# Optimization experiments

Hardware: AMD Instinct MI355X
Metric: run time of the kernel (lower is better)

## Reference

```python
import jax, jax.numpy as jnp
import numpy as np

B, S, D_MODEL, H = 2, 2048, 768, 12
HD = D_MODEL // H  # head_dim = 64
EPS = 1e-5


def setup_inputs() -> dict:
    key = jax.random.key(0)
    ks = jax.random.split(key, 5)
    sc = 0.02
    return {
        "x": jax.random.normal(ks[0], (B, S, D_MODEL), dtype=jnp.float32),
        "Wproj_w": jax.random.normal(ks[1], (7 * D_MODEL, D_MODEL), dtype=jnp.float32) * sc,
        "Wproj_b": jax.random.normal(ks[2], (7 * D_MODEL,), dtype=jnp.float32) * sc,
        "gn_w": jnp.ones((D_MODEL,), dtype=jnp.float32),
        "gn_b": jnp.zeros((D_MODEL,), dtype=jnp.float32),
        "out_w": jax.random.normal(ks[3], (D_MODEL, D_MODEL), dtype=jnp.float32) * sc,
        "out_b": jax.random.normal(ks[4], (D_MODEL,), dtype=jnp.float32) * sc,
    }


def _time_swiglu(qkv):
    # qkv: [B, S, 7, H, D]
    q1, k1, q2, k2, q3, k3, v = [qkv[:, :, i] for i in range(7)]
    a1 = jnp.einsum('bthd,bshd->bhts', q1, k1)  # [B,H,S,S], raw scores, no softmax
    a2 = jnp.einsum('bthd,bshd->bhts', q2, k2)
    a3 = jnp.einsum('bthd,bshd->bhts', q3, k3)
    t1 = jax.nn.silu(jnp.einsum('bhts,bshd->bthd', a1, v))
    t2 = jnp.einsum('bhts,bshd->bthd', a2, v)
    return jnp.einsum('bhts,bshd->bthd', a3, t1 * t2)  # [B,S,H,D]


def _group_norm(ctx, gn_w, gn_b):
    # ctx: [B, S, D_MODEL]; torch applies GroupNorm(H, D_MODEL) over (B, C=D_MODEL, L=S)
    g = ctx.reshape(B, S, H, HD)
    mean = jnp.mean(g, axis=(1, 3), keepdims=True)          # per (batch, group) over (S, HD)
    var = jnp.var(g, axis=(1, 3), keepdims=True)
    g = (g - mean) * jax.lax.rsqrt(var + EPS)
    g = g.reshape(B, S, D_MODEL)
    return g * gn_w + gn_b


def reference(x, Wproj_w, Wproj_b, gn_w, gn_b, out_w, out_b):
    qkv = x @ Wproj_w.T + Wproj_b                  # [B,S,7*D_MODEL]
    qkv = qkv.reshape(B, S, 7, H, HD)
    ctx = _time_swiglu(qkv).reshape(B, S, D_MODEL)  # [B,S,D_MODEL]
    ctx = _group_norm(ctx, gn_w, gn_b)
    return ctx @ out_w.T + out_b
```

## Files before the change

kernel.cpp:

```cpp
#include <hip/hip_runtime.h>
#include <hip/hip_bf16.h>
#include <stdint.h>

typedef short short8 __attribute__((ext_vector_type(8)));
typedef float f32x4 __attribute__((ext_vector_type(4)));
typedef float f32x16 __attribute__((ext_vector_type(16)));
typedef unsigned short u16x4 __attribute__((ext_vector_type(4)));
typedef unsigned uint4v __attribute__((ext_vector_type(4)));

#define MFMA16 __builtin_amdgcn_mfma_f32_16x16x32_bf16
#define MFMA32 __builtin_amdgcn_mfma_f32_32x32x16_bf16

typedef unsigned int __attribute__((address_space(1))) as1_u32;
typedef unsigned int __attribute__((address_space(3))) as3_u32;
#define GLOAD16(gsrc, ldst) \
  __builtin_amdgcn_global_load_lds((const as1_u32*)(gsrc), (as3_u32*)(ldst), 16, 0, 0)

__device__ __forceinline__ unsigned short f2bf(float f) {
  __hip_bfloat16 h = __float2bfloat16(f);
  return *(unsigned short*)&h;
}
__device__ __forceinline__ unsigned pk2(float lo, float hi) {
  return ((unsigned)f2bf(hi) << 16) | (unsigned)f2bf(lo);
}
__device__ __forceinline__ void plswap(unsigned &a, unsigned &b) {
  asm volatile("v_permlane32_swap_b32 %0, %1" : "+v"(a), "+v"(b));
}

__device__ __forceinline__ short8 pv_frag(const f32x16* acc, int kc2) {
  int n = kc2 >> 1, c = kc2 & 1;
  int o0 = 2 * c, o1 = 2 * c + 1;
  unsigned x0 = pk2(acc[n][o0 * 4 + 0], acc[n][o0 * 4 + 1]);
  unsigned x1 = pk2(acc[n][o0 * 4 + 2], acc[n][o0 * 4 + 3]);
  unsigned y0 = pk2(acc[n][o1 * 4 + 0], acc[n][o1 * 4 + 1]);
  unsigned y1 = pk2(acc[n][o1 * 4 + 2], acc[n][o1 * 4 + 3]);
  plswap(x0, y0);
  plswap(x1, y1);
  uint4v fu; fu.x = x0; fu.y = x1; fu.z = y0; fu.w = y1;
  return __builtin_bit_cast(short8, fu);
}

__global__ __launch_bounds__(256) void cvt_bf16_4(const float* __restrict__ in,
                                                  unsigned short* __restrict__ out,
                                                  int n) {
  int i = (blockIdx.x * 256 + threadIdx.x) * 4;
  if (i >= n) return;
  f32x4 v = *(const f32x4*)(in + i);
  u16x4 o;
  o.x = f2bf(v.x); o.y = f2bf(v.y); o.z = f2bf(v.z); o.w = f2bf(v.w);
  *(u16x4*)(out + i) = o;
}

__global__ __launch_bounds__(256) void transp64(const unsigned short* __restrict__ src,
                                                int stride, int off,
                                                unsigned short* __restrict__ dst) {
  __shared__ __align__(16) unsigned short t[64 * 64];
  const int tid = threadIdx.x;
  const int tt = blockIdx.x, bh = blockIdx.y;
  const int b = bh / 12, h = bh % 12;
  const unsigned short* sbase = src + (size_t)(b * 2048 + tt * 64) * stride + h * 64 + off;
  for (int it = 0; it < 2; ++it) {
    int slot = it * 256 + tid, s = slot >> 3, j = slot & 7;
    short8 v = *(const short8*)(sbase + (size_t)s * stride + j * 8);
    int phys = (s + 8 * j) & 63;
    for (int e = 0; e < 8; ++e)
      t[(j * 8 + e) * 64 + phys] = ((unsigned short*)&v)[e];
  }
  __syncthreads();
  unsigned short* dbase = dst + (size_t)bh * 64 * 2048 + tt * 64;
  for (int it = 0; it < 2; ++it) {
    int slot = it * 256 + tid, d = slot >> 3, c = slot & 7;
    int pc = (c + (d >> 3)) & 7;
    short8 v = *(const short8*)(t + d * 64 + pc * 8);
    *(short8*)(dbase + (size_t)d * 2048 + c * 8) = v;
  }
}

template <bool OUT_BF16>
__global__ __launch_bounds__(256) void gemm_nt(const unsigned short* __restrict__ A,
                                               const unsigned short* __restrict__ Bm,
                                               const float* __restrict__ bias,
                                               void* __restrict__ Cout,
                                               int M, int N, int K) {
  __shared__ __align__(16) char smem[32768];
  char* As = smem;
  char* Bs = smem + 16384;
  const int tid = threadIdx.x;
  const int w = tid >> 6, l = tid & 63;
  const int wm = w >> 1, wn = w & 1;
  const int Row0 = blockIdx.y * 128, Col0 = blockIdx.x * 128;

  f32x4 z; z.x = 0.f; z.y = 0.f; z.z = 0.f; z.w = 0.f;
  f32x4 acc[4][4];
  for (int m = 0; m < 4; ++m)
    for (int n = 0; n < 4; ++n) acc[m][n] = z;

  for (int k0 = 0; k0 < K; k0 += 64) {
    for (int it = 0; it < 4; ++it) {
      int slot = it * 256 + tid;
      int row = slot >> 3, j = slot & 7;
      int gc = j ^ (row & 7);
      GLOAD16(A + (size_t)(Row0 + row) * K + k0 + gc * 8, As + slot * 16);
      GLOAD16(Bm + (size_t)(Col0 + row) * K + k0 + gc * 8, Bs + slot * 16);
    }
    __syncthreads();
    for (int kc = 0; kc < 2; ++kc) {
      int c = (l >> 4) + 4 * kc;
      short8 af[4], bf[4];
      for (int m = 0; m < 4; ++m) {
        int t = wm * 64 + m * 16 + (l & 15);
        af[m] = *(const short8*)(As + t * 128 + ((c ^ (t & 7)) * 16));
      }
      for (int n = 0; n < 4; ++n) {
        int t = wn * 64 + n * 16 + (l & 15);
        bf[n] = *(const short8*)(Bs + t * 128 + ((c ^ (t & 7)) * 16));
      }
      for (int m = 0; m < 4; ++m)
        for (int n = 0; n < 4; ++n)
          acc[m][n] = MFMA16(af[m], bf[n], acc[m][n], 0, 0, 0);
    }
    __syncthreads();
  }
  for (int n = 0; n < 4; ++n) {
    int col = Col0 + wn * 64 + n * 16 + (l & 15);
    float bv = bias[col];
    for (int m = 0; m < 4; ++m) {
      int rbase = Row0 + wm * 64 + m * 16 + (l >> 4) * 4;
      for (int r = 0; r < 4; ++r) {
        float v = acc[m][n][r] + bv;
        size_t idx = (size_t)(rbase + r) * N + col;
        if (OUT_BF16) ((unsigned short*)Cout)[idx] = f2bf(v);
        else          ((float*)Cout)[idx] = v;
      }
    }
  }
}

__global__ __launch_bounds__(256) void pass1(const unsigned short* __restrict__ qkv,
                                             const unsigned short* __restrict__ vt,
                                             unsigned short* __restrict__ u) {
  __shared__ __align__(16) char smem[49152];
  const int tid = threadIdx.x, w = tid >> 6, l = tid & 63;
  const int m = w & 1, sh = w >> 1;
  const int g5 = l >> 5, l31 = l & 31;
  const int tt = blockIdx.x, bh = blockIdx.y;
  const int b = bh / 12, h = bh % 12;

  short8 qf[2][4];
#pragma unroll
  for (int tb = 0; tb < 2; ++tb) {
    const unsigned short* qrow =
        qkv + (size_t)(b * 2048 + tt * 64 + tb * 32 + l31) * 5376 + h * 64 + m * 2 * 768;
#pragma unroll
    for (int kc = 0; kc < 4; ++kc)
      qf[tb][kc] = *(const short8*)(qrow + kc * 16 + g5 * 8);
  }

  f32x16 z16;
#pragma unroll
  for (int i = 0; i < 16; ++i) z16[i] = 0.f;
  f32x16 tacc[2][2];
  tacc[0][0] = z16; tacc[0][1] = z16; tacc[1][0] = z16; tacc[1][1] = z16;

  auto STAGE = [&](char* buf, int si) {
#pragma unroll
    for (int shs = 0; shs < 2; ++shs) {
      int s0 = shs * 1024 + si * 32;
      char* hb = buf + shs * 12288;
      {
        int row = tid >> 3, pc = tid & 7, gc = pc ^ (row & 7);
        const unsigned short* base =
            qkv + (size_t)(b * 2048 + s0 + row) * 5376 + h * 64 + gc * 8;
        GLOAD16(base + 768, hb + tid * 16);
        GLOAD16(base + 3 * 768, hb + 4096 + tid * 16);
      }
      {
        int row = tid >> 2, pc = tid & 3, gc = pc ^ ((row >> 1) & 3);
        GLOAD16(vt + (size_t)(bh * 64 + row) * 2048 + s0 + gc * 8,
                hb + 8192 + tid * 16);
      }
    }
  };

  STAGE(smem, 0);
  __syncthreads();
  for (int si = 0; si < 32; ++si) {
    const char* cur = smem + (si & 1) * 24576 + sh * 12288;
    if (si < 31) STAGE(smem + ((si + 1) & 1) * 24576, si + 1);
    const char* Ks = cur + m * 4096;
    const char* Vs = cur + 8192;

    short8 kreg[4], vreg[4];
#pragma unroll
    for (int kc = 0; kc < 4; ++kc)
      kreg[kc] = *(const short8*)(Ks + l31 * 128 + (((kc * 2 + g5) ^ (l31 & 7)) * 16));
#pragma unroll
    for (int kc2 = 0; kc2 < 2; ++kc2)
#pragma unroll
      for (int dn = 0; dn < 2; ++dn) {
        int drow = dn * 32 + l31, c = kc2 * 2 + g5;
        vreg[kc2 * 2 + dn] =
            *(const short8*)(Vs + drow * 64 + ((c ^ ((drow >> 1) & 3)) * 16));
      }

#pragma unroll
    for (int tb = 0; tb < 2; ++tb) {
      f32x16 a = z16;
#pragma unroll
      for (int kc = 0; kc < 4; ++kc)
        a = MFMA32(kreg[kc], qf[tb][kc], a, 0, 0, 0);
#pragma unroll
      for (int kc2 = 0; kc2 < 2; ++kc2) {
        short8 pa = pv_frag(&a, kc2);
#pragma unroll
        for (int dn = 0; dn < 2; ++dn)
          tacc[tb][dn] = MFMA32(pa, vreg[kc2 * 2 + dn], tacc[tb][dn], 0, 0, 0);
      }
    }
    __syncthreads();
  }

  float* ex = (float*)smem;
  if (sh == 1) {
#pragma unroll
    for (int tb = 0; tb < 2; ++tb)
#pragma unroll
      for (int dn = 0; dn < 2; ++dn)
#pragma unroll
        for (int qd = 0; qd < 4; ++qd) {
          f32x4 v;
          v.x = tacc[tb][dn][qd * 4 + 0]; v.y = tacc[tb][dn][qd * 4 + 1];
          v.z = tacc[tb][dn][qd * 4 + 2]; v.w = tacc[tb][dn][qd * 4 + 3];
          *(f32x4*)((char*)ex + m * 16384 + ((tb * 2 + dn) * 4 + qd) * 1024 + l * 16) = v;
        }
  }
  __syncthreads();
  if (sh == 0) {
#pragma unroll
    for (int tb = 0; tb < 2; ++tb)
#pragma unroll
      for (int dn = 0; dn < 2; ++dn)
#pragma unroll
        for (int qd = 0; qd < 4; ++qd) {
          f32x4 v = *(const f32x4*)((char*)ex + m * 16384 +
                                    ((tb * 2 + dn) * 4 + qd) * 1024 + l * 16);
          tacc[tb][dn][qd * 4 + 0] += v.x; tacc[tb][dn][qd * 4 + 1] += v.y;
          tacc[tb][dn][qd * 4 + 2] += v.z; tacc[tb][dn][qd * 4 + 3] += v.w;
        }
  }
  __syncthreads();
  if (sh == 0 && m == 1) {
#pragma unroll
    for (int tb = 0; tb < 2; ++tb)
#pragma unroll
      for (int dn = 0; dn < 2; ++dn)
#pragma unroll
        for (int qd = 0; qd < 4; ++qd) {
          f32x4 v;
          v.x = tacc[tb][dn][qd * 4 + 0]; v.y = tacc[tb][dn][qd * 4 + 1];
          v.z = tacc[tb][dn][qd * 4 + 2]; v.w = tacc[tb][dn][qd * 4 + 3];
          *(f32x4*)((char*)ex + ((tb * 2 + dn) * 4 + qd) * 1024 + l * 16) = v;
        }
  }
  __syncthreads();
  if (sh == 0 && m == 0) {
#pragma unroll
    for (int tb = 0; tb < 2; ++tb)
#pragma unroll
      for (int dn = 0; dn < 2; ++dn)
#pragma unroll
        for (int r = 0; r < 16; ++r) {
          float x2 = ex[((tb * 2 + dn) * 4 + (r >> 2)) * 256 + l * 4 + (r & 3)];
          int t = tt * 64 + tb * 32 + (r & 3) + 8 * (r >> 2) + 4 * g5;
          int d = dn * 32 + l31;
          float x1 = tacc[tb][dn][r];
          float uu = (x1 / (1.f + expf(-x1))) * x2;
          u[(size_t)(b * 2048 + t) * 768 + h * 64 + d] = f2bf(uu);
        }
  }
}

__global__ __launch_bounds__(256) void pass2(const unsigned short* __restrict__ qkv,
                                             const unsigned short* __restrict__ ut,
                                             float* __restrict__ ctx,
                                             float* __restrict__ partials) {
  __shared__ __align__(16) char smem[32768];
  const int tid = threadIdx.x, w = tid >> 6, l = tid & 63;
  const int g5 = l >> 5, l31 = l & 31;
  const int tt = blockIdx.x, bh = blockIdx.y;
  const int b = bh / 12, h = bh % 12;

  short8 qf[2][4];
#pragma unroll
  for (int tb = 0; tb < 2; ++tb) {
    const unsigned short* qrow =
        qkv + (size_t)(b * 2048 + tt * 64 + tb * 32 + l31) * 5376 + h * 64 + 4 * 768;
#pragma unroll
    for (int kc = 0; kc < 4; ++kc)
      qf[tb][kc] = *(const short8*)(qrow + kc * 16 + g5 * 8);
  }

  f32x16 z16;
#pragma unroll
  for (int i = 0; i < 16; ++i) z16[i] = 0.f;
  f32x16 ca[2][2];
  ca[0][0] = z16; ca[0][1] = z16; ca[1][0] = z16; ca[1][1] = z16;

  auto STAGE = [&](int si) {
#pragma unroll
    for (int qs = 0; qs < 4; ++qs) {
      int s0 = qs * 512 + si * 32;
      char* hb = smem + qs * 8192;
      {
        int row = tid >> 3, pc = tid & 7, gc = pc ^ (row & 7);
        GLOAD16(qkv + (size_t)(b * 2048 + s0 + row) * 5376 + h * 64 + 5 * 768 + gc * 8,
                hb + tid * 16);
      }
      {
        int row = tid >> 2, pc = tid & 3, gc = pc ^ ((row >> 1) & 3);
        GLOAD16(ut + (size_t)(bh * 64 + row) * 2048 + s0 + gc * 8,
                hb + 4096 + tid * 16);
      }
    }
  };

  for (int si = 0; si < 16; ++si) {
    STAGE(si);
    __syncthreads();
    const char* Ks = smem + w * 8192;
    const char* Us = Ks + 4096;

    short8 kreg[4], ureg[4];
#pragma unroll
    for (int kc = 0; kc < 4; ++kc)
      kreg[kc] = *(const short8*)(Ks + l31 * 128 + (((kc * 2 + g5) ^ (l31 & 7)) * 16));
#pragma unroll
    for (int kc2 = 0; kc2 < 2; ++kc2)
#pragma unroll
      for (int dn = 0; dn < 2; ++dn) {
        int drow = dn * 32 + l31, c = kc2 * 2 + g5;
        ureg[kc2 * 2 + dn] =
            *(const short8*)(Us + drow * 64 + ((c ^ ((drow >> 1) & 3)) * 16));
      }

#pragma unroll
    for (int tb = 0; tb < 2; ++tb) {
      f32x16 a = z16;
#pragma unroll
      for (int kc = 0; kc < 4; ++kc)
        a = MFMA32(kreg[kc], qf[tb][kc], a, 0, 0, 0);
#pragma unroll
      for (int kc2 = 0; kc2 < 2; ++kc2) {
        short8 pa = pv_frag(&a, kc2);
#pragma unroll
        for (int dn = 0; dn < 2; ++dn)
          ca[tb][dn] = MFMA32(pa, ureg[kc2 * 2 + dn], ca[tb][dn], 0, 0, 0);
      }
    }
    __syncthreads();
  }

  float* ex = (float*)smem;
  auto DUMP = [&](int region) {
#pragma unroll
    for (int tb = 0; tb < 2; ++tb)
#pragma unroll
      for (int dn = 0; dn < 2; ++dn)
#pragma unroll
        for (int qd = 0; qd < 4; ++qd) {
          f32x4 v;
          v.x = ca[tb][dn][qd * 4 + 0]; v.y = ca[tb][dn][qd * 4 + 1];
          v.z = ca[tb][dn][qd * 4 + 2]; v.w = ca[tb][dn][qd * 4 + 3];
          *(f32x4*)((char*)ex + region * 16384 + ((tb * 2 + dn) * 4 + qd) * 1024 + l * 16) = v;
        }
  };
  auto ACCUM = [&](int region) {
#pragma unroll
    for (int tb = 0; tb < 2; ++tb)
#pragma unroll
      for (int dn = 0; dn < 2; ++dn)
#pragma unroll
        for (int qd = 0; qd < 4; ++qd) {
          f32x4 v = *(const f32x4*)((char*)ex + region * 16384 +
                                    ((tb * 2 + dn) * 4 + qd) * 1024 + l * 16);
          ca[tb][dn][qd * 4 + 0] += v.x; ca[tb][dn][qd * 4 + 1] += v.y;
          ca[tb][dn][qd * 4 + 2] += v.z; ca[tb][dn][qd * 4 + 3] += v.w;
        }
  };
  if (w == 1) DUMP(0);
  if (w == 3) DUMP(1);
  __syncthreads();
  if (w == 0) ACCUM(0);
  if (w == 2) ACCUM(1);
  __syncthreads();
  if (w == 2) DUMP(0);
  __syncthreads();
  float psum = 0.f, psum2 = 0.f;
  if (w == 0) {
    ACCUM(0);
#pragma unroll
    for (int tb = 0; tb < 2; ++tb)
#pragma unroll
      for (int dn = 0; dn < 2; ++dn)
#pragma unroll
        for (int r = 0; r < 16; ++r) {
          int t = tt * 64 + tb * 32 + (r & 3) + 8 * (r >> 2) + 4 * g5;
          int d = dn * 32 + l31;
          float v = ca[tb][dn][r];
          ctx[(size_t)(b * 2048 + t) * 768 + h * 64 + d] = v;
          psum += v; psum2 += v * v;
        }
    for (int off = 32; off > 0; off >>= 1) {
      psum += __shfl_down(psum, off, 64);
      psum2 += __shfl_down(psum2, off, 64);
    }
    if (l == 0) {
      partials[(bh * 32 + tt) * 2] = psum;
      partials[(bh * 32 + tt) * 2 + 1] = psum2;
    }
  }
}

__global__ __launch_bounds__(64) void gn_finalize(const float* __restrict__ partials,
                                                  float* __restrict__ stats) {
  const int g = blockIdx.x;
  const int l = threadIdx.x;
  double s = 0.0, s2 = 0.0;
  if (l < 32) {
    s = (double)partials[(g * 32 + l) * 2];
    s2 = (double)partials[(g * 32 + l) * 2 + 1];
  }
  for (int off = 32; off > 0; off >>= 1) {
    s += __shfl_down(s, off, 64);
    s2 += __shfl_down(s2, off, 64);
  }
  if (l == 0) {
    const double N = 2048.0 * 64.0;
    double mean = s / N;
    double var = s2 / N - mean * mean;
    stats[g * 2] = (float)mean;
    stats[g * 2 + 1] = (float)(1.0 / sqrt(var + 1e-5));
  }
}

__global__ __launch_bounds__(256) void gn_apply(const float* __restrict__ ctx,
                                                const float* __restrict__ stats,
                                                const float* __restrict__ gw,
                                                const float* __restrict__ gb,
                                                unsigned short* __restrict__ outc) {
  int i = blockIdx.x * 256 + threadIdx.x;
  if (i >= 4096 * 768) return;
  int c = i % 768;
  int b = i / (2048 * 768);
  int g = b * 12 + (c >> 6);
  float v = (ctx[i] - stats[2 * g]) * stats[2 * g + 1];
  outc[i] = f2bf(v * gw[c] + gb[c]);
}

extern "C" void kernel_launch(void* const* d_in, const int* in_sizes, int n_in,
                              void* d_out, int out_size, void* d_ws, size_t ws_size,
                              hipStream_t stream) {
  const float* x   = (const float*)d_in[0];
  const float* Wpw = (const float*)d_in[1];
  const float* Wpb = (const float*)d_in[2];
  const float* gnw = (const float*)d_in[3];
  const float* gnb = (const float*)d_in[4];
  const float* ow  = (const float*)d_in[5];
  const float* ob  = (const float*)d_in[6];
  float* out = (float*)d_out;

  char* ws = (char*)d_ws;
  size_t off = 0;
  auto carve = [&](size_t bytes) {
    char* p = ws + off;
    off = (off + bytes + 255) & ~(size_t)255;
    return p;
  };
  unsigned short* xb   = (unsigned short*)carve((size_t)4096 * 768 * 2);
  unsigned short* wb   = (unsigned short*)carve((size_t)5376 * 768 * 2);
  unsigned short* owb  = (unsigned short*)carve((size_t)768 * 768 * 2);
  unsigned short* qkvb = (unsigned short*)carve((size_t)4096 * 5376 * 2);
  unsigned short* ub   = (unsigned short*)carve((size_t)4096 * 768 * 2);
  unsigned short* vtb  = (unsigned short*)carve((size_t)24 * 64 * 2048 * 2);
  unsigned short* utb  = (unsigned short*)carve((size_t)24 * 64 * 2048 * 2);
  float* ctx           = (float*)carve((size_t)4096 * 768 * 4);
  float* partials      = (float*)carve(24 * 32 * 2 * 4);
  float* stats         = (float*)carve(48 * 4);

  cvt_bf16_4<<<3072, 256, 0, stream>>>(x, xb, 4096 * 768);
  cvt_bf16_4<<<4032, 256, 0, stream>>>(Wpw, wb, 5376 * 768);
  cvt_bf16_4<<<576, 256, 0, stream>>>(ow, owb, 768 * 768);

  gemm_nt<true><<<dim3(42, 32), 256, 0, stream>>>(xb, wb, Wpb, qkvb, 4096, 5376, 768);
  transp64<<<dim3(32, 24), 256, 0, stream>>>(qkvb, 5376, 6 * 768, vtb);
  pass1<<<dim3(32, 24), 256, 0, stream>>>(qkvb, vtb, ub);
  transp64<<<dim3(32, 24), 256, 0, stream>>>(ub, 768, 0, utb);
  pass2<<<dim3(32, 24), 256, 0, stream>>>(qkvb, utb, ctx, partials);
  gn_finalize<<<24, 64, 0, stream>>>(partials, stats);
  gn_apply<<<12288, 256, 0, stream>>>(ctx, stats, gnw, gnb, xb);
  gemm_nt<false><<<dim3(6, 32), 256, 0, stream>>>(xb, owb, ob, out, 4096, 768, 768);
}
```

Baseline: 227.4 us.

## Double-buffer pass2 staging, hoist load pointers, swizzle GEMM tiles, raise MFMA priority

Pass2 gets a double-buffered LDS stage of 64KB, so global-to-LDS loads for the next chunk overlap compute on the current one instead of waiting on a synchronous load. Both attention passes now advance precomputed pointers rather than recomputing addresses on each stage. They also wrap the MFMA section in s_setprio. The GEMM remaps block indices with an 8-way swizzle to improve L2 locality. The larger LDS footprint may lower pass2 occupancy, and the swizzle assumes the block count divides by 8.

```diff
diff --git a/kernel.cpp b/kernel.cpp
--- a/kernel.cpp
+++ b/kernel.cpp
@@ -88,7 +88,11 @@
   const int tid = threadIdx.x;
   const int w = tid >> 6, l = tid & 63;
   const int wm = w >> 1, wn = w & 1;
-  const int Row0 = blockIdx.y * 128, Col0 = blockIdx.x * 128;
+  const int gx = gridDim.x;
+  const int lin = blockIdx.y * gx + blockIdx.x;
+  const int cpx = (gx * gridDim.y) >> 3;
+  const int swz = (lin & 7) * cpx + (lin >> 3);
+  const int Row0 = (swz / gx) * 128, Col0 = (swz % gx) * 128;
 
   f32x4 z; z.x = 0.f; z.y = 0.f; z.z = 0.f; z.w = 0.f;
   f32x4 acc[4][4];
@@ -162,31 +166,30 @@
   f32x16 tacc[2][2];
   tacc[0][0] = z16; tacc[0][1] = z16; tacc[1][0] = z16; tacc[1][1] = z16;
 
-  auto STAGE = [&](char* buf, int si) {
-#pragma unroll
-    for (int shs = 0; shs < 2; ++shs) {
-      int s0 = shs * 1024 + si * 32;
-      char* hb = buf + shs * 12288;
-      {
-        int row = tid >> 3, pc = tid & 7, gc = pc ^ (row & 7);
-        const unsigned short* base =
-            qkv + (size_t)(b * 2048 + s0 + row) * 5376 + h * 64 + gc * 8;
-        GLOAD16(base + 768, hb + tid * 16);
-        GLOAD16(base + 3 * 768, hb + 4096 + tid * 16);
-      }
-      {
-        int row = tid >> 2, pc = tid & 3, gc = pc ^ ((row >> 1) & 3);
-        GLOAD16(vt + (size_t)(bh * 64 + row) * 2048 + s0 + gc * 8,
-                hb + 8192 + tid * 16);
-      }
-    }
+  const unsigned short *k1p0, *k1p1, *vtp0, *vtp1;
+  {
+    int row = tid >> 3, pc = tid & 7, gc = pc ^ (row & 7);
+    k1p0 = qkv + (size_t)(b * 2048 + row) * 5376 + h * 64 + 768 + gc * 8;
+    k1p1 = k1p0 + (size_t)1024 * 5376;
+    int rowv = tid >> 2, pcv = tid & 3, gcv = pcv ^ ((rowv >> 1) & 3);
+    vtp0 = vt + (size_t)(bh * 64 + rowv) * 2048 + gcv * 8;
+    vtp1 = vtp0 + 1024;
+  }
+  auto STAGE = [&](char* buf) {
+    GLOAD16(k1p0, buf + tid * 16);
+    GLOAD16(k1p0 + 1536, buf + 4096 + tid * 16);
+    GLOAD16(vtp0, buf + 8192 + tid * 16);
+    GLOAD16(k1p1, buf + 12288 + tid * 16);
+    GLOAD16(k1p1 + 1536, buf + 12288 + 4096 + tid * 16);
+    GLOAD16(vtp1, buf + 12288 + 8192 + tid * 16);
+    k1p0 += 32 * 5376; k1p1 += 32 * 5376; vtp0 += 32; vtp1 += 32;
   };
 
-  STAGE(smem, 0);
+  STAGE(smem);
   __syncthreads();
   for (int si = 0; si < 32; ++si) {
     const char* cur = smem + (si & 1) * 24576 + sh * 12288;
-    if (si < 31) STAGE(smem + ((si + 1) & 1) * 24576, si + 1);
+    if (si < 31) STAGE(smem + ((si + 1) & 1) * 24576);
     const char* Ks = cur + m * 4096;
     const char* Vs = cur + 8192;
 
@@ -203,6 +206,7 @@
             *(const short8*)(Vs + drow * 64 + ((c ^ ((drow >> 1) & 3)) * 16));
       }
 
+    __builtin_amdgcn_s_setprio(1);
 #pragma unroll
     for (int tb = 0; tb < 2; ++tb) {
       f32x16 a = z16;
@@ -217,6 +221,7 @@
           tacc[tb][dn] = MFMA32(pa, vreg[kc2 * 2 + dn], tacc[tb][dn], 0, 0, 0);
       }
     }
+    __builtin_amdgcn_s_setprio(0);
     __syncthreads();
   }
 
@@ -284,7 +289,7 @@
                                              const unsigned short* __restrict__ ut,
                                              float* __restrict__ ctx,
                                              float* __restrict__ partials) {
-  __shared__ __align__(16) char smem[32768];
+  __shared__ __align__(16) char smem[65536];
   const int tid = threadIdx.x, w = tid >> 6, l = tid & 63;
   const int g5 = l >> 5, l31 = l & 31;
   const int tt = blockIdx.x, bh = blockIdx.y;
@@ -306,28 +311,36 @@
   f32x16 ca[2][2];
   ca[0][0] = z16; ca[0][1] = z16; ca[1][0] = z16; ca[1][1] = z16;
 
-  auto STAGE = [&](int si) {
-#pragma unroll
-    for (int qs = 0; qs < 4; ++qs) {
-      int s0 = qs * 512 + si * 32;
-      char* hb = smem + qs * 8192;
-      {
-        int row = tid >> 3, pc = tid & 7, gc = pc ^ (row & 7);
-        GLOAD16(qkv + (size_t)(b * 2048 + s0 + row) * 5376 + h * 64 + 5 * 768 + gc * 8,
-                hb + tid * 16);
-      }
-      {
-        int row = tid >> 2, pc = tid & 3, gc = pc ^ ((row >> 1) & 3);
-        GLOAD16(ut + (size_t)(bh * 64 + row) * 2048 + s0 + gc * 8,
-                hb + 4096 + tid * 16);
-      }
-    }
+  const unsigned short *kp0, *kp1, *kp2, *kp3, *up0, *up1, *up2, *up3;
+  {
+    int row = tid >> 3, pc = tid & 7, gc = pc ^ (row & 7);
+    kp0 = qkv + (size_t)(b * 2048 + row) * 5376 + h * 64 + 5 * 768 + gc * 8;
+    kp1 = kp0 + (size_t)512 * 5376;
+    kp2 = kp1 + (size_t)512 * 5376;
+    kp3 = kp2 + (size_t)512 * 5376;
+    int rowv = tid >> 2, pcv = tid & 3, gcv = pcv ^ ((rowv >> 1) & 3);
+    up0 = ut + (size_t)(bh * 64 + rowv) * 2048 + gcv * 8;
+    up1 = up0 + 512; up2 = up1 + 512; up3 = up2 + 512;
+  }
+  auto STAGE = [&](char* buf) {
+    GLOAD16(kp0, buf + tid * 16);
+    GLOAD16(up0, buf + 4096 + tid * 16);
+    GLOAD16(kp1, buf + 8192 + tid * 16);
+    GLOAD16(up1, buf + 12288 + tid * 16);
+    GLOAD16(kp2, buf + 16384 + tid * 16);
+    GLOAD16(up2, buf + 20480 + tid * 16);
+    GLOAD16(kp3, buf + 24576 + tid * 16);
+    GLOAD16(up3, buf + 28672 + tid * 16);
+    kp0 += 32 * 5376; kp1 += 32 * 5376; kp2 += 32 * 5376; kp3 += 32 * 5376;
+    up0 += 32; up1 += 32; up2 += 32; up3 += 32;
   };
 
+  STAGE(smem);
+  __syncthreads();
   for (int si = 0; si < 16; ++si) {
-    STAGE(si);
-    __syncthreads();
-    const char* Ks = smem + w * 8192;
+    const char* cur = smem + (si & 1) * 32768;
+    if (si < 15) STAGE(smem + ((si + 1) & 1) * 32768);
+    const char* Ks = cur + w * 8192;
     const char* Us = Ks + 4096;
 
     short8 kreg[4], ureg[4];
@@ -343,6 +356,7 @@
             *(const short8*)(Us + drow * 64 + ((c ^ ((drow >> 1) & 3)) * 16));
       }
 
+    __builtin_amdgcn_s_setprio(1);
 #pragma unroll
     for (int tb = 0; tb < 2; ++tb) {
       f32x16 a = z16;
@@ -357,6 +371,7 @@
           ca[tb][dn] = MFMA32(pa, ureg[kc2 * 2 + dn], ca[tb][dn], 0, 0, 0);
       }
     }
+    __builtin_amdgcn_s_setprio(0);
     __syncthreads();
   }
 
```

New measurement: 226.0 us. No clear change (-0.6%).
